# Performance work log

Measured on AMD Instinct MI355X. Metric: run time of the kernel, lower is better.

Reference implementation:

```python
import math
import jax, jax.numpy as jnp
import numpy as np

B = 1024
D = 384
Q = 65536
TOPK = 128
HARD_W = 2.0
TEMP_START = 0.2
TEMP_END = 0.05
WARMUP = 10


def _temperature(epoch):
    # curriculum cosine decay (epoch is a Python int)
    if epoch >= WARMUP:
        return TEMP_END
    progress = epoch / max(1, WARMUP)
    return TEMP_END + 0.5 * (TEMP_START - TEMP_END) * (1.0 + math.cos(math.pi * progress))


def _normalize(x):
    # F.normalize: x / max(||x||, eps)
    n = jnp.linalg.norm(x, axis=-1, keepdims=True)
    return x / jnp.maximum(n, 1e-12)


def _hard_neg_reweight(logits):
    # logits: [B, N]; labels = arange(B) (diagonal positives)
    b = logits.shape[0]
    rows = jnp.arange(b)
    neg_logits = logits.at[rows, rows].set(-jnp.inf)      # mask positives
    _, hard_idx = jax.lax.top_k(neg_logits, TOPK)          # [B, TOPK] hardest negatives
    weights = jnp.ones_like(logits)
    weights = weights.at[rows[:, None], hard_idx].set(HARD_W)
    weights = weights.at[rows, rows].set(1.0)
    return logits * weights


def _cross_entropy_diag(logits):
    b = logits.shape[0]
    logp = jax.nn.log_softmax(logits, axis=-1)
    return -jnp.mean(logp[jnp.arange(b), jnp.arange(b)])


def setup_inputs() -> dict:
    key = jax.random.key(0)
    k1, k2, k3, k4 = jax.random.split(key, 4)
    rgb_feat = jax.random.normal(k1, (B, D), dtype=jnp.float32)
    ir_feat = jax.random.normal(k2, (B, D), dtype=jnp.float32)
    rgb_queue = _normalize(jax.random.normal(k3, (Q, D), dtype=jnp.float32))
    ir_queue = _normalize(jax.random.normal(k4, (Q, D), dtype=jnp.float32))
    return {"rgb_feat": rgb_feat, "ir_feat": ir_feat,
            "rgb_queue": rgb_queue, "ir_queue": ir_queue, "epoch": 0}


def reference(rgb_feat, ir_feat, rgb_queue, ir_queue, epoch):
    temp = _temperature(epoch)
    rgb_z = _normalize(rgb_feat.astype(jnp.float32))
    ir_z = _normalize(ir_feat.astype(jnp.float32))
    ir_all = jnp.concatenate([ir_z, ir_queue], axis=0)    # [B+Q, D]
    rgb_all = jnp.concatenate([rgb_z, rgb_queue], axis=0)
    logits_r2i = (rgb_z @ ir_all.T) / temp                # [B, B+Q]
    logits_i2r = (ir_z @ rgb_all.T) / temp
    logits_r2i = _hard_neg_reweight(logits_r2i)
    logits_i2r = _hard_neg_reweight(logits_i2r)
    return 0.5 * (_cross_entropy_diag(logits_r2i) + _cross_entropy_diag(logits_i2r))
```

## Files before the change

### kernel.cpp

```cpp
#include <hip/hip_runtime.h>
#include <hip/hip_bf16.h>

#define B_    1024
#define D_    384
#define Q_    65536
#define N_    66560
#define TOPK_ 128

#define NBIN_ 4096
#define CAP_  2048

typedef __bf16 bf16x8 __attribute__((ext_vector_type(8)));
typedef float  f32x4  __attribute__((ext_vector_type(4)));
typedef unsigned short u16;
typedef u16 u16x8 __attribute__((ext_vector_type(8)));

__device__ __forceinline__ unsigned short f2bf(float x) {
  unsigned int u = __float_as_uint(x);
  unsigned int r = (u + 0x7fffu + ((u >> 16) & 1u)) >> 16;
  return (unsigned short)r;
}

__device__ __forceinline__ void gld_lds16(const void* g, void* l) {
  __builtin_amdgcn_global_load_lds(
      (__attribute__((address_space(1))) void*)(g),
      (__attribute__((address_space(3))) void*)(l), 16, 0, 0);
}

__device__ __forceinline__ unsigned int bf2key(unsigned int u) {
  return u ^ ((u & 0x8000u) ? 0xFFFFu : 0x8000u);
}

__global__ __launch_bounds__(64) void k_normalize(
    const float* __restrict__ rgb, const float* __restrict__ ir,
    const int* __restrict__ ep,
    u16* __restrict__ zrA, u16* __restrict__ ziA,
    u16* __restrict__ zrU, u16* __restrict__ ziU)
{
  int r = blockIdx.x & (B_ - 1);
  bool isIr = blockIdx.x >= B_;
  const float* src = (isIr ? ir : rgb) + (size_t)r * D_;
  u16* dA = (isIr ? ziA : zrA) + (size_t)r * D_;
  u16* dU = (isIr ? ziU : zrU) + (size_t)r * D_;
  int t = threadIdx.x;
  float x[6]; float ss = 0.f;
  #pragma unroll
  for (int k = 0; k < 6; ++k) { x[k] = src[t + 64*k]; ss += x[k]*x[k]; }
  #pragma unroll
  for (int off = 32; off > 0; off >>= 1) ss += __shfl_down(ss, off);
  ss = __shfl(ss, 0);
  float inv = 1.0f / fmaxf(sqrtf(ss), 1e-12f);

  int e = ep[0];
  float temp;
  if (e >= 10) temp = 0.05f;
  else {
    float p = (float)e * 0.1f;
    temp = 0.05f + 0.075f * (1.0f + cosf(3.14159265358979323846f * p));
  }
  float itemp = 1.0f / temp;

  #pragma unroll
  for (int k = 0; k < 6; ++k) {
    float z = x[k] * inv;
    dU[t + 64*k] = f2bf(z);
    dA[t + 64*k] = f2bf(z * itemp);
  }
}

__global__ __launch_bounds__(256) void k_build_ball(
    const u16* __restrict__ zU, const float* __restrict__ queue,
    u16* __restrict__ ball)
{
  size_t i = ((size_t)blockIdx.x * 256 + threadIdx.x) * 8;
  const size_t zElems = (size_t)B_ * D_;
  if (i < zElems) {
    *(uint4*)(ball + i) = *(const uint4*)(zU + i);
  } else {
    const float* q = queue + (i - zElems);
    float4 a = *(const float4*)q;
    float4 b = *(const float4*)(q + 4);
    u16x8 o;
    o[0] = f2bf(a.x); o[1] = f2bf(a.y); o[2] = f2bf(a.z); o[3] = f2bf(a.w);
    o[4] = f2bf(b.x); o[5] = f2bf(b.y); o[6] = f2bf(b.z); o[7] = f2bf(b.w);
    *(u16x8*)(ball + i) = o;
  }
}

#define BK_ 64
#define NSTEP_ 6
__global__ __launch_bounds__(256) void k_gemm(
    const u16* __restrict__ A,
    const u16* __restrict__ ball,
    u16* __restrict__ C,
    float* __restrict__ diag,
    int r0, int mtiles)
{
  __shared__ __align__(16) unsigned char smem[65536];
  u16* AsBuf[2] = { (u16*)smem,           (u16*)(smem + 32768) };
  u16* BsBuf[2] = { (u16*)(smem + 16384), (u16*)(smem + 49152) };
  u16* Ct = (u16*)smem;

  int bid = blockIdx.x;
  int nwg = gridDim.x;
  int cpx = nwg >> 3;
  int wgid = (bid & 7) * cpx + (bid >> 3);
  int nt = wgid / mtiles;
  int mt = wgid - nt * mtiles;

  const int tid  = threadIdx.x;
  const int wave = tid >> 6, lane = tid & 63;
  const int wm = wave >> 1, wn = wave & 1;
  const int mbase = mt * 128;
  const int nbase = nt * 128;
  const u16* Ab = A    + (size_t)(r0 + mbase) * D_;
  const u16* Bb = ball + (size_t)nbase * D_;

  const int rr0 = tid >> 3;
  const int c0  = tid & 7;
  const int koff = (((c0 * 16) ^ ((rr0 & 7) << 4)) >> 1);

  f32x4 acc[4][4];
  #pragma unroll
  for (int m = 0; m < 4; ++m)
    #pragma unroll
    for (int n = 0; n < 4; ++n)
      #pragma unroll
      for (int r = 0; r < 4; ++r) acc[m][n][r] = 0.0f;

  const int lr = lane & 15, lk = (lane >> 4) * 8;

  #pragma unroll
  for (int i = 0; i < 4; ++i) {
    int f = i * 256 + tid;
    int rr = rr0 + i * 32;
    gld_lds16(Ab + (size_t)rr * D_ + koff, AsBuf[0] + (size_t)f * 8);
    gld_lds16(Bb + (size_t)rr * D_ + koff, BsBuf[0] + (size_t)f * 8);
  }
  __syncthreads();

  #pragma unroll
  for (int t = 0; t < NSTEP_; ++t) {
    const int cur = t & 1;
    u16* Ac = AsBuf[cur];
    u16* Bc = BsBuf[cur];
    if (t + 1 < NSTEP_) {
      const int nxt = cur ^ 1;
      const int ks = (t + 1) * BK_;
      #pragma unroll
      for (int i = 0; i < 4; ++i) {
        int f = i * 256 + tid;
        int rr = rr0 + i * 32;
        gld_lds16(Ab + (size_t)rr * D_ + ks + koff, AsBuf[nxt] + (size_t)f * 8);
        gld_lds16(Bb + (size_t)rr * D_ + ks + koff, BsBuf[nxt] + (size_t)f * 8);
      }
    }
    #pragma unroll
    for (int kk = 0; kk < BK_; kk += 32) {
      bf16x8 af[4], bq[4];
      const int kb = (kk + lk) * 2;
      #pragma unroll
      for (int m = 0; m < 4; ++m) {
        int row = wm*64 + m*16 + lr;
        af[m] = *(const bf16x8*)((const char*)Ac + row * 128 + (kb ^ ((row & 7) << 4)));
      }
      #pragma unroll
      for (int n = 0; n < 4; ++n) {
        int row = wn*64 + n*16 + lr;
        bq[n] = *(const bf16x8*)((const char*)Bc + row * 128 + (kb ^ ((row & 7) << 4)));
      }
      #pragma unroll
      for (int m = 0; m < 4; ++m)
        #pragma unroll
        for (int n = 0; n < 4; ++n)
          acc[m][n] = __builtin_amdgcn_mfma_f32_16x16x32_bf16(af[m], bq[n], acc[m][n], 0, 0, 0);
    }
    __syncthreads();
  }

  const int rowq = (lane >> 4) * 4;
  #pragma unroll
  for (int m = 0; m < 4; ++m) {
    #pragma unroll
    for (int n = 0; n < 4; ++n) {
      int lcol = wn*64 + n*16 + lr;
      int gcol = nbase + lcol;
      #pragma unroll
      for (int r = 0; r < 4; ++r) {
        int lrow = wm*64 + m*16 + rowq + r;
        float x = acc[m][n][r];
        int grow = r0 + mbase + lrow;
        if (gcol == grow) { diag[grow] = x; x = -60.0f; }
        Ct[lrow * 136 + lcol] = f2bf(x);
      }
    }
  }
  __syncthreads();

  int rrow = tid >> 4;
  int cchunk = (tid & 15) * 8;
  #pragma unroll
  for (int pass = 0; pass < 8; ++pass) {
    int row = pass * 16 + rrow;
    u16x8 v = *(const u16x8*)(Ct + row * 136 + cchunk);
    *(u16x8*)(C + (size_t)(mbase + row) * N_ + nbase + cchunk) = v;
  }
}

__global__ __launch_bounds__(256) void k_select(
    const u16* __restrict__ C, const float* __restrict__ diag,
    float* __restrict__ rowloss, int r0)
{
  __shared__ unsigned int hist[NBIN_];
  __shared__ float vals[CAP_];
  __shared__ float fred[256];
  __shared__ unsigned int csum[256];
  __shared__ int sh_bstar, sh_above, sh_cnt;

  const int t = threadIdx.x;
  const int grow = r0 + blockIdx.x;
  const u16x8* p = (const u16x8*)(C + (size_t)blockIdx.x * N_);

  uint4* h4 = (uint4*)hist;
  #pragma unroll
  for (int i = 0; i < 4; ++i) h4[i * 256 + t] = make_uint4(0,0,0,0);
  if (t == 0) sh_cnt = 0;
  __syncthreads();

  float es0 = 0.f, es1 = 0.f;
  #pragma unroll 1
  for (int base = 0; base < 8192; base += 2048) {
    u16x8 v[8];
    #pragma unroll
    for (int j = 0; j < 8; ++j) v[j] = p[base + j * 256 + t];
    #pragma unroll
    for (int j = 0; j < 8; ++j) {
      #pragma unroll
      for (int e = 0; e < 8; ++e) {
        unsigned int u = (unsigned int)(unsigned short)v[j][e];
        atomicAdd(&hist[bf2key(u) >> 4], 1u);
        float ex = __expf(__uint_as_float(u << 16));
        if (j & 1) es1 += ex; else es0 += ex;
      }
    }
  }
  if (t < 128) {
    u16x8 v = p[8192 + t];
    #pragma unroll
    for (int e = 0; e < 8; ++e) {
      unsigned int u = (unsigned int)(unsigned short)v[e];
      atomicAdd(&hist[bf2key(u) >> 4], 1u);
      es0 += __expf(__uint_as_float(u << 16));
    }
  }
  float esum = es0 + es1;
  __syncthreads();

  unsigned int S = 0;
  #pragma unroll
  for (int i = 0; i < 16; ++i) S += hist[t * 16 + i];
  csum[t] = S;
  __syncthreads();

  unsigned int a = S;
  #pragma unroll
  for (int s = 1; s < 256; s <<= 1) {
    unsigned int add = (t + s < 256) ? csum[t + s] : 0u;
    __syncthreads();
    a += add; csum[t] = a;
    __syncthreads();
  }

  int above_chunk = (t < 255) ? (int)csum[t + 1] : 0;
  if (above_chunk < TOPK_ && above_chunk + (int)S >= TOPK_) {
    int cum = above_chunk;
    #pragma unroll 1
    for (int i = 15; i >= 0; --i) {
      int c = (int)hist[t * 16 + i];
      if (cum + c >= TOPK_) { sh_bstar = t * 16 + i; sh_above = cum; break; }
      cum += c;
    }
  }
  __syncthreads();
  const unsigned int bstar = (unsigned int)sh_bstar;
  const int A = sh_above;

  float delta = 0.f;
  #pragma unroll 1
  for (int base = 0; base < 8192; base += 2048) {
    u16x8 v[8];
    #pragma unroll
    for (int j = 0; j < 8; ++j) v[j] = p[base + j * 256 + t];
    #pragma unroll
    for (int j = 0; j < 8; ++j) {
      #pragma unroll
      for (int e = 0; e < 8; ++e) {
        unsigned int u = (unsigned int)(unsigned short)v[j][e];
        unsigned int bin = bf2key(u) >> 4;
        if (bin >= bstar) {
          float val = __uint_as_float(u << 16);
          if (bin > bstar) delta += __expf(2.f * val) - __expf(val);
          else { int s = atomicAdd(&sh_cnt, 1); if (s < CAP_) vals[s] = val; }
        }
      }
    }
  }
  if (t < 128) {
    u16x8 v = p[8192 + t];
    #pragma unroll
    for (int e = 0; e < 8; ++e) {
      unsigned int u = (unsigned int)(unsigned short)v[e];
      unsigned int bin = bf2key(u) >> 4;
      if (bin >= bstar) {
        float val = __uint_as_float(u << 16);
        if (bin > bstar) delta += __expf(2.f * val) - __expf(val);
        else { int s = atomicAdd(&sh_cnt, 1); if (s < CAP_) vals[s] = val; }
      }
    }
  }
  __syncthreads();

  int C2 = sh_cnt < CAP_ ? sh_cnt : CAP_;
  int need = TOPK_ - A;
  for (int i = t; i < C2; i += 256) {
    float v = vals[i];
    int g = 0;
    for (int k = 0; k < C2; ++k)
      g += (vals[k] > v) || (vals[k] == v && k < i);
    if (g < need) delta += __expf(2.f * v) - __expf(v);
  }

  fred[t] = esum + delta;
  __syncthreads();
  #pragma unroll
  for (int s = 128; s > 0; s >>= 1) { if (t < s) fred[t] += fred[t + s]; __syncthreads(); }

  if (t == 0) {
    float d = diag[grow];
    rowloss[grow] = logf(fred[0] + __expf(d)) - d;
  }
}

__global__ __launch_bounds__(256) void k_final(
    const float* __restrict__ rowloss, float* __restrict__ out)
{
  __shared__ float red[256];
  int t = threadIdx.x;
  float s = 0.f;
  for (int i = t; i < 2 * B_; i += 256) s += rowloss[i];
  red[t] = s;
  __syncthreads();
  for (int k = 128; k > 0; k >>= 1) { if (t < k) red[t] += red[t + k]; __syncthreads(); }
  if (t == 0) out[0] = red[0] * (1.0f / (2.0f * B_));
}

extern "C" void kernel_launch(void* const* d_in, const int* in_sizes, int n_in,
                              void* d_out, int out_size, void* d_ws, size_t ws_size,
                              hipStream_t stream)
{
  const float* rgb_feat = (const float*)d_in[0];
  const float* ir_feat  = (const float*)d_in[1];
  const float* rgb_q    = (const float*)d_in[2];
  const float* ir_q     = (const float*)d_in[3];
  const int*   epoch    = (const int*)d_in[4];

  char* ws = (char*)d_ws;
  size_t off = 0;
  auto alloc = [&](size_t bytes) -> char* {
    char* p = ws + off;
    off = (off + bytes + 255) & ~(size_t)255;
    return p;
  };

  u16* zrA = (u16*)alloc((size_t)B_ * D_ * 2);
  u16* ziA = (u16*)alloc((size_t)B_ * D_ * 2);
  u16* zrU = (u16*)alloc((size_t)B_ * D_ * 2);
  u16* ziU = (u16*)alloc((size_t)B_ * D_ * 2);
  float* diag    = (float*)alloc((size_t)2 * B_ * 4);
  float* rowloss = (float*)alloc((size_t)2 * B_ * 4);
  u16* ball = (u16*)alloc((size_t)N_ * D_ * 2);

  size_t avail = ws_size > off ? ws_size - off : 0;
  int SR = (int)(avail / ((size_t)N_ * 2));
  SR &= ~127;
  if (SR > B_) SR = B_;
  if (SR < 128) SR = 128;
  u16* slab = (u16*)(ws + off);

  k_normalize<<<dim3(2 * B_), dim3(64), 0, stream>>>(
      rgb_feat, ir_feat, epoch, zrA, ziA, zrU, ziU);

  for (int dir = 0; dir < 2; ++dir) {
    const u16*   Amat   = (dir == 0) ? zrA : ziA;
    const u16*   zOther = (dir == 0) ? ziU : zrU;
    const float* queue  = (dir == 0) ? ir_q : rgb_q;
    float* diagD = diag    + dir * B_;
    float* lossD = rowloss + dir * B_;

    k_build_ball<<<dim3((unsigned)((size_t)N_ * D_ / 8 / 256)), dim3(256), 0, stream>>>(
        zOther, queue, ball);

    for (int r0 = 0; r0 < B_; r0 += SR) {
      int cur = (B_ - r0) < SR ? (B_ - r0) : SR;
      int mtiles = cur / 128;
      int nwg = (N_ / 128) * mtiles;
      k_gemm<<<dim3(nwg), dim3(256), 0, stream>>>(
          Amat, ball, slab, diagD, r0, mtiles);
      k_select<<<dim3(cur), dim3(256), 0, stream>>>(slab, diagD, lossD, r0);
    }
  }

  k_final<<<dim3(1), dim3(256), 0, stream>>>(rowloss, (float*)d_out);
}
```

Before: 336.6 us.

## Deepen GEMM K-pipeline to four LDS stages with explicit vmcnt waits

Replaces the double-buffered BK=64 GEMM main loop with a four-stage ring of BK=32 tiles, issuing loads three steps ahead and using manual s_waitcnt vmcnt and raw barriers instead of __syncthreads. The LDS swizzle is adjusted for the 64-byte row pitch, and launch bounds request two blocks per CU. The aim is to hide global-to-LDS latency behind MFMA work. In exchange there are twice as many barriers per tile, and the hand-written vmcnt counts depend on exactly four loads per stage.

```diff
diff --git a/kernel.cpp b/kernel.cpp
--- a/kernel.cpp
+++ b/kernel.cpp
@@ -25,6 +25,15 @@
   __builtin_amdgcn_global_load_lds(
       (__attribute__((address_space(1))) void*)(g),
       (__attribute__((address_space(3))) void*)(l), 16, 0, 0);
+}
+
+__device__ __forceinline__ void wait_vmcnt(int n) {
+  switch (n) {
+    case 12: asm volatile("s_waitcnt vmcnt(12)" ::: "memory"); break;
+    case 8:  asm volatile("s_waitcnt vmcnt(8)"  ::: "memory"); break;
+    case 4:  asm volatile("s_waitcnt vmcnt(4)"  ::: "memory"); break;
+    default: asm volatile("s_waitcnt vmcnt(0)"  ::: "memory"); break;
+  }
 }
 
 __device__ __forceinline__ unsigned int bf2key(unsigned int u) {
@@ -87,9 +96,9 @@
   }
 }
 
-#define BK_ 64
-#define NSTEP_ 6
-__global__ __launch_bounds__(256) void k_gemm(
+#define BK_ 32
+#define NSTEP_ 12
+__global__ __launch_bounds__(256, 2) void k_gemm(
     const u16* __restrict__ A,
     const u16* __restrict__ ball,
     u16* __restrict__ C,
@@ -97,8 +106,6 @@
     int r0, int mtiles)
 {
   __shared__ __align__(16) unsigned char smem[65536];
-  u16* AsBuf[2] = { (u16*)smem,           (u16*)(smem + 32768) };
-  u16* BsBuf[2] = { (u16*)(smem + 16384), (u16*)(smem + 49152) };
   u16* Ct = (u16*)smem;
 
   int bid = blockIdx.x;
@@ -116,9 +123,19 @@
   const u16* Ab = A    + (size_t)(r0 + mbase) * D_;
   const u16* Bb = ball + (size_t)nbase * D_;
 
-  const int rr0 = tid >> 3;
-  const int c0  = tid & 7;
-  const int koff = (((c0 * 16) ^ ((rr0 & 7) << 4)) >> 1);
+  auto As = [&](int t) -> u16* { return (u16*)(smem + (t & 3) * 8192); };
+  auto Bs = [&](int t) -> u16* { return (u16*)(smem + 32768 + (t & 3) * 8192); };
+  auto stage = [&](int t) {
+    const int ks = t * BK_;
+    #pragma unroll
+    for (int i = 0; i < 2; ++i) {
+      int f = i * 256 + tid;
+      int rr = f >> 2, cc = f & 3;
+      int koff = (((cc * 16) ^ (((rr >> 1) & 3) << 4)) >> 1);
+      gld_lds16(Ab + (size_t)rr * D_ + ks + koff, As(t) + (size_t)f * 8);
+      gld_lds16(Bb + (size_t)rr * D_ + ks + koff, Bs(t) + (size_t)f * 8);
+    }
+  };
 
   f32x4 acc[4][4];
   #pragma unroll
@@ -128,54 +145,40 @@
       #pragma unroll
       for (int r = 0; r < 4; ++r) acc[m][n][r] = 0.0f;
 
-  const int lr = lane & 15, lk = (lane >> 4) * 8;
-
-  #pragma unroll
-  for (int i = 0; i < 4; ++i) {
-    int f = i * 256 + tid;
-    int rr = rr0 + i * 32;
-    gld_lds16(Ab + (size_t)rr * D_ + koff, AsBuf[0] + (size_t)f * 8);
-    gld_lds16(Bb + (size_t)rr * D_ + koff, BsBuf[0] + (size_t)f * 8);
-  }
-  __syncthreads();
+  const int lr = lane & 15;
+  const int kb = (lane >> 4) * 16;
+
+  stage(0); stage(1); stage(2);
 
   #pragma unroll
   for (int t = 0; t < NSTEP_; ++t) {
-    const int cur = t & 1;
-    u16* Ac = AsBuf[cur];
-    u16* Bc = BsBuf[cur];
-    if (t + 1 < NSTEP_) {
-      const int nxt = cur ^ 1;
-      const int ks = (t + 1) * BK_;
+    if (t + 3 < NSTEP_) stage(t + 3);
+    wait_vmcnt(t < NSTEP_ - 3 ? 12 : (NSTEP_ - 1 - t) * 4);
+    __builtin_amdgcn_s_barrier();
+    __builtin_amdgcn_sched_barrier(0);
+
+    const u16* Ac = As(t);
+    const u16* Bc = Bs(t);
+    bf16x8 af[4], bq[4];
+    #pragma unroll
+    for (int m = 0; m < 4; ++m) {
+      int row = wm*64 + m*16 + lr;
+      af[m] = *(const bf16x8*)((const char*)Ac + row * 64 + (kb ^ (((row >> 1) & 3) << 4)));
+    }
+    #pragma unroll
+    for (int n = 0; n < 4; ++n) {
+      int row = wn*64 + n*16 + lr;
+      bq[n] = *(const bf16x8*)((const char*)Bc + row * 64 + (kb ^ (((row >> 1) & 3) << 4)));
+    }
+    #pragma unroll
+    for (int m = 0; m < 4; ++m)
       #pragma unroll
-      for (int i = 0; i < 4; ++i) {
-        int f = i * 256 + tid;
-        int rr = rr0 + i * 32;
-        gld_lds16(Ab + (size_t)rr * D_ + ks + koff, AsBuf[nxt] + (size_t)f * 8);
-        gld_lds16(Bb + (size_t)rr * D_ + ks + koff, BsBuf[nxt] + (size_t)f * 8);
-      }
-    }
-    #pragma unroll
-    for (int kk = 0; kk < BK_; kk += 32) {
-      bf16x8 af[4], bq[4];
-      const int kb = (kk + lk) * 2;
-      #pragma unroll
-      for (int m = 0; m < 4; ++m) {
-        int row = wm*64 + m*16 + lr;
-        af[m] = *(const bf16x8*)((const char*)Ac + row * 128 + (kb ^ ((row & 7) << 4)));
-      }
-      #pragma unroll
-      for (int n = 0; n < 4; ++n) {
-        int row = wn*64 + n*16 + lr;
-        bq[n] = *(const bf16x8*)((const char*)Bc + row * 128 + (kb ^ ((row & 7) << 4)));
-      }
-      #pragma unroll
-      for (int m = 0; m < 4; ++m)
-        #pragma unroll
-        for (int n = 0; n < 4; ++n)
-          acc[m][n] = __builtin_amdgcn_mfma_f32_16x16x32_bf16(af[m], bq[n], acc[m][n], 0, 0, 0);
-    }
-    __syncthreads();
+      for (int n = 0; n < 4; ++n)
+        acc[m][n] = __builtin_amdgcn_mfma_f32_16x16x32_bf16(af[m], bq[n], acc[m][n], 0, 0, 0);
+
+    asm volatile("s_waitcnt lgkmcnt(0)" ::: "memory");
+    __builtin_amdgcn_sched_barrier(0);
+    __builtin_amdgcn_s_barrier();
   }
 
   const int rowq = (lane >> 4) * 4;
```

Measured after the change: 318.1 us, median of 2. 5.5% less time.
